# Optimization experiments

Measured on AMD Instinct MI355X. Metric: run time of the kernel, lower is better.

## Reference

```python
import jax, jax.numpy as jnp
import numpy as np

EPS = 1e-8  # torch CosineSimilarity default eps

def setup_inputs() -> dict:
    key = jax.random.key(0)
    kv, kt, k1, k2, k3, k4 = jax.random.split(key, 6)
    B, S = 16, 1024
    VD, TD, H = 1024, 768, 512
    visual_features = jax.random.normal(kv, (B, S, VD), dtype=jnp.float32)
    text_features = jax.random.normal(kt, (B, S, TD), dtype=jnp.float32)
    # nn.Linear params: weight [out, in], bias [out]
    Wv = jax.random.normal(k1, (H, VD), dtype=jnp.float32) * (1.0 / np.sqrt(VD))
    bv = jax.random.normal(k2, (H,), dtype=jnp.float32) * 0.01
    Wt = jax.random.normal(k3, (H, TD), dtype=jnp.float32) * (1.0 / np.sqrt(TD))
    bt = jax.random.normal(k4, (H,), dtype=jnp.float32) * 0.01
    return {"visual_features": visual_features, "text_features": text_features,
            "Wv": Wv, "bv": bv, "Wt": Wt, "bt": bt}

def reference(visual_features, text_features, Wv, bv, Wt, bt):
    # Linear projections
    v = jnp.einsum('bsd,hd->bsh', visual_features, Wv) + bv  # [B,S,H]
    t = jnp.einsum('bsd,hd->bsh', text_features, Wt) + bt    # [B,S,H]
    # Cosine similarity matrix via normalized batched GEMM
    # (algebraically equal to broadcasting CosineSimilarity over (B,S,S,H))
    dots = jnp.einsum('bih,bjh->bij', v, t)                   # [B,S,S]
    vn = jnp.linalg.norm(v, axis=-1)                          # [B,S]
    tn = jnp.linalg.norm(t, axis=-1)                          # [B,S]
    denom = jnp.maximum(vn[:, :, None] * tn[:, None, :], EPS)
    return dots / denom
```

## Files before the change

kernel.cpp:

```cpp
#include <hip/hip_runtime.h>
#include <hip/hip_bf16.h>

typedef __bf16 bf16x8 __attribute__((ext_vector_type(8)));
typedef __bf16 bf16x4 __attribute__((ext_vector_type(4)));
typedef float  f32x4  __attribute__((ext_vector_type(4)));

#define MFMA16(a, b, c) __builtin_amdgcn_mfma_f32_16x16x32_bf16((a), (b), (c), 0, 0, 0)

#define BATCH 16
#define SEQ   1024
#define VD    1024
#define TD    768
#define HDIM  512
#define MROWS (BATCH * SEQ)

typedef __attribute__((address_space(1))) const unsigned int gas_uint;
typedef __attribute__((address_space(3))) unsigned int las_uint;

__device__ __forceinline__ void async_copy16(const void* g, void* l) {
    __builtin_amdgcn_global_load_lds((gas_uint*)g, (las_uint*)l, 16, 0, 0);
}

__global__ __launch_bounds__(256) void wconv_kernel(const float* __restrict__ Wv,
                                                    const float* __restrict__ Wt,
                                                    __bf16* __restrict__ Wbv,
                                                    __bf16* __restrict__ Wbt) {
    const int NV = (HDIM * VD) / 4;
    const int NT = (HDIM * TD) / 4;
    int i = blockIdx.x * 256 + threadIdx.x;
    const float* src;
    __bf16* dst;
    if (i < NV) { src = Wv; dst = Wbv; }
    else        { i -= NV; if (i >= NT) return; src = Wt; dst = Wbt; }
    const float4 x = reinterpret_cast<const float4*>(src)[i];
    bf16x4 p = {(__bf16)x.x, (__bf16)x.y, (__bf16)x.z, (__bf16)x.w};
    reinterpret_cast<bf16x4*>(dst)[i] = p;
}

__global__ __launch_bounds__(256) void proj_kernel(
    const float* __restrict__ Xv, const __bf16* __restrict__ Wbv, const float* __restrict__ bv_,
    const float* __restrict__ Xt, const __bf16* __restrict__ Wbt, const float* __restrict__ bt_,
    __bf16* __restrict__ vout, __bf16* __restrict__ tout,
    float* __restrict__ vn2, float* __restrict__ tn2)
{
    const int L     = blockIdx.x;
    const int mlow  = L & 7;
    const int n     = (L >> 3) & 3;
    const int mhigh = (L >> 5) & 15;
    const int z     = L >> 9;
    const int m0    = (mhigh * 8 + mlow) * 128;
    const int n0    = n * 128;

    const float* X; const __bf16* Wb; const float* bias; __bf16* out; float* n2; int K;
    if (z == 0) { X = Xv; Wb = Wbv; bias = bv_; out = vout; n2 = vn2; K = VD; }
    else        { X = Xt; Wb = Wbt; bias = bt_; out = tout; n2 = tn2; K = TD; }

    __shared__ float  As[128 * 32];
    __shared__ __bf16 Bs[128 * 32];

    const int tid  = threadIdx.x;
    const int lane = tid & 63;
    const int wave = tid >> 6;
    const int wr   = wave >> 1;
    const int wc   = wave & 1;
    const int fr   = lane & 15;
    const int fq   = lane >> 4;

    f32x4 acc[4][4] = {};

    const int nk = K >> 5;
    for (int ki = 0; ki < nk; ++ki) {
        const int kk = ki << 5;

#pragma unroll
        for (int i = 0; i < 4; ++i) {
            const int c = i * 256 + tid;
            const int r = c >> 3;
            const int g = (c & 7) ^ (r & 7);
            async_copy16(&X[(size_t)(m0 + r) * K + kk + g * 4], &As[(c & ~63) * 4]);
        }
#pragma unroll
        for (int i = 0; i < 2; ++i) {
            const int c = i * 256 + tid;
            const int r = c >> 2;
            const int g = (c & 3) ^ (r & 3);
            async_copy16(&Wb[(size_t)(n0 + r) * K + kk + g * 8], &Bs[(c & ~63) * 8]);
        }
        __syncthreads();

        bf16x8 a[4], b[4];
#pragma unroll
        for (int tm = 0; tm < 4; ++tm) {
            const int r   = wr * 64 + tm * 16 + fr;
            const int key = r & 7;
            const f32x4 lo = *reinterpret_cast<const f32x4*>(&As[(r * 8 + ((fq * 2)     ^ key)) * 4]);
            const f32x4 hi = *reinterpret_cast<const f32x4*>(&As[(r * 8 + ((fq * 2 + 1) ^ key)) * 4]);
            bf16x8 av = {(__bf16)lo[0], (__bf16)lo[1], (__bf16)lo[2], (__bf16)lo[3],
                         (__bf16)hi[0], (__bf16)hi[1], (__bf16)hi[2], (__bf16)hi[3]};
            a[tm] = av;
        }
#pragma unroll
        for (int tn = 0; tn < 4; ++tn) {
            const int r = wc * 64 + tn * 16 + fr;
            b[tn] = *reinterpret_cast<const bf16x8*>(&Bs[(r * 4 + (fq ^ (r & 3))) * 8]);
        }
#pragma unroll
        for (int tm = 0; tm < 4; ++tm)
#pragma unroll
            for (int tn = 0; tn < 4; ++tn)
                acc[tm][tn] = MFMA16(a[tm], b[tn], acc[tm][tn]);
        __syncthreads();
    }

    float bc[4];
#pragma unroll
    for (int tn = 0; tn < 4; ++tn)
        bc[tn] = bias[n0 + wc * 64 + tn * 16 + fr];

#pragma unroll
    for (int tm = 0; tm < 4; ++tm) {
        const int rowb = m0 + wr * 64 + tm * 16 + fq * 4;
#pragma unroll
        for (int r = 0; r < 4; ++r) {
            float s = 0.f;
#pragma unroll
            for (int tn = 0; tn < 4; ++tn) {
                const float e = acc[tm][tn][r] + bc[tn];
                out[(size_t)(rowb + r) * HDIM + n0 + wc * 64 + tn * 16 + fr] = (__bf16)e;
                s = fmaf(e, e, s);
            }
            s += __shfl_xor(s, 1);
            s += __shfl_xor(s, 2);
            s += __shfl_xor(s, 4);
            s += __shfl_xor(s, 8);
            if (fr == 0) atomicAdd(&n2[rowb + r], s);
        }
    }
}

__global__ __launch_bounds__(256) void dots_kernel(const __bf16* __restrict__ v,
                                                   const __bf16* __restrict__ t,
                                                   const float* __restrict__ vn2,
                                                   const float* __restrict__ tn2,
                                                   float* __restrict__ out) {
    __shared__ __bf16 As[128 * 32];
    __shared__ __bf16 Bs[128 * 32];

    const int L  = blockIdx.x;
    const int b  = (L & 7) + ((L >> 9) << 3);
    const int j0 = ((L >> 3) & 7) * 128;
    const int i0 = ((L >> 6) & 7) * 128;

    const __bf16* vb = v + (size_t)b * SEQ * HDIM;
    const __bf16* tb = t + (size_t)b * SEQ * HDIM;

    const int tid  = threadIdx.x;
    const int lane = tid & 63;
    const int wave = tid >> 6;
    const int wr   = wave >> 1;
    const int wc   = wave & 1;
    const int fr   = lane & 15;
    const int fq   = lane >> 4;

    f32x4 acc[4][4] = {};

    for (int kk = 0; kk < HDIM; kk += 32) {
#pragma unroll
        for (int s = 0; s < 2; ++s) {
            const int c    = (wave * 2 + s) * 64 + lane;
            const int row  = c >> 2;
            const int part = c & 3;
            async_copy16(&vb[(size_t)(i0 + row) * HDIM + kk + part * 8],
                         &As[(wave * 2 + s) * 512]);
            async_copy16(&tb[(size_t)(j0 + row) * HDIM + kk + part * 8],
                         &Bs[(wave * 2 + s) * 512]);
        }
        __syncthreads();

        bf16x8 a[4], bfr[4];
#pragma unroll
        for (int t_ = 0; t_ < 4; ++t_) {
            a[t_]   = *reinterpret_cast<const bf16x8*>(&As[(wr * 64 + t_ * 16 + fr) * 32 + fq * 8]);
            bfr[t_] = *reinterpret_cast<const bf16x8*>(&Bs[(wc * 64 + t_ * 16 + fr) * 32 + fq * 8]);
        }
#pragma unroll
        for (int tm = 0; tm < 4; ++tm)
#pragma unroll
            for (int tn_ = 0; tn_ < 4; ++tn_)
                acc[tm][tn_] = MFMA16(a[tm], bfr[tn_], acc[tm][tn_]);
        __syncthreads();
    }

    float vr2[16];
#pragma unroll
    for (int tm = 0; tm < 4; ++tm)
#pragma unroll
        for (int r = 0; r < 4; ++r)
            vr2[tm * 4 + r] = vn2[b * SEQ + i0 + wr * 64 + tm * 16 + fq * 4 + r];

    float* outb = out + ((size_t)b << 20);
#pragma unroll
    for (int tn_ = 0; tn_ < 4; ++tn_) {
        const int j     = j0 + wc * 64 + tn_ * 16 + fr;
        const float tj2 = tn2[b * SEQ + j];
#pragma unroll
        for (int tm = 0; tm < 4; ++tm) {
            const int ib = i0 + wr * 64 + tm * 16 + fq * 4;
#pragma unroll
            for (int r = 0; r < 4; ++r) {
                const float denom = fmaxf(sqrtf(vr2[tm * 4 + r] * tj2), 1e-8f);
                outb[(size_t)(ib + r) * SEQ + j] = acc[tm][tn_][r] * __builtin_amdgcn_rcpf(denom);
            }
        }
    }
}

extern "C" void kernel_launch(void* const* d_in, const int* in_sizes, int n_in,
                              void* d_out, int out_size, void* d_ws, size_t ws_size,
                              hipStream_t stream) {
    const float* Xv = (const float*)d_in[0];
    const float* Xt = (const float*)d_in[1];
    const float* Wv = (const float*)d_in[2];
    const float* bv = (const float*)d_in[3];
    const float* Wt = (const float*)d_in[4];
    const float* bt = (const float*)d_in[5];
    float* out = (float*)d_out;

    char* ws = (char*)d_ws;
    size_t off = 0;
    __bf16* v   = (__bf16*)(ws + off); off += (size_t)MROWS * HDIM * 2;
    __bf16* t   = (__bf16*)(ws + off); off += (size_t)MROWS * HDIM * 2;
    __bf16* Wbv = (__bf16*)(ws + off); off += (size_t)HDIM * VD * 2;
    __bf16* Wbt = (__bf16*)(ws + off); off += (size_t)HDIM * TD * 2;
    float*  vn2 = (float*)(ws + off);  off += (size_t)MROWS * 4;
    float*  tn2 = (float*)(ws + off);  off += (size_t)MROWS * 4;

    hipMemsetAsync(vn2, 0, (size_t)2 * MROWS * 4, stream);

    wconv_kernel<<<896, 256, 0, stream>>>(Wv, Wt, Wbv, Wbt);

    proj_kernel<<<1024, 256, 0, stream>>>(Xv, Wbv, bv, Xt, Wbt, bt, v, t, vn2, tn2);

    dots_kernel<<<1024, 256, 0, stream>>>(v, t, vn2, tn2, out);
}
```

Baseline: 260.8 us.

## Pre-convert activations to bf16 and double-buffer GEMM tiles with BK=64

```diff
diff --git a/kernel.cpp b/kernel.cpp
--- a/kernel.cpp
+++ b/kernel.cpp
@@ -21,25 +21,51 @@
     __builtin_amdgcn_global_load_lds((gas_uint*)g, (las_uint*)l, 16, 0, 0);
 }
 
-__global__ __launch_bounds__(256) void wconv_kernel(const float* __restrict__ Wv,
-                                                    const float* __restrict__ Wt,
-                                                    __bf16* __restrict__ Wbv,
-                                                    __bf16* __restrict__ Wbt) {
-    const int NV = (HDIM * VD) / 4;
-    const int NT = (HDIM * TD) / 4;
+__device__ __forceinline__ void stage_tile_bf16(const __bf16* __restrict__ src,
+                                                size_t ld, int row0, int k0,
+                                                __bf16* __restrict__ buf, int tid) {
+#pragma unroll
+    for (int i = 0; i < 4; ++i) {
+        const int c = i * 256 + tid;
+        const int r = c >> 3;
+        const int g = (c & 7) ^ (r & 7);
+        async_copy16(&src[(size_t)(row0 + r) * ld + k0 + g * 8],
+                     &buf[(c & ~63) * 8]);
+    }
+}
+
+__device__ __forceinline__ bf16x8 frag_read(const __bf16* __restrict__ buf,
+                                            int r, int h, int fq) {
+    return *reinterpret_cast<const bf16x8*>(&buf[(r * 8 + ((h * 4 + fq) ^ (r & 7))) * 8]);
+}
+
+#define NC_XV (BATCH * SEQ * VD / 4)
+#define NC_XT (BATCH * SEQ * TD / 4)
+#define NC_WV (HDIM * VD / 4)
+#define NC_WT (HDIM * TD / 4)
+#define NC_TOTAL (NC_XV + NC_XT + NC_WV + NC_WT)
+
+__global__ __launch_bounds__(256) void conv_kernel(
+    const float* __restrict__ Xv, const float* __restrict__ Xt,
+    const float* __restrict__ Wv, const float* __restrict__ Wt,
+    __bf16* __restrict__ Xvb, __bf16* __restrict__ Xtb,
+    __bf16* __restrict__ Wvb, __bf16* __restrict__ Wtb) {
     int i = blockIdx.x * 256 + threadIdx.x;
+    if (i >= NC_TOTAL) return;
     const float* src;
     __bf16* dst;
-    if (i < NV) { src = Wv; dst = Wbv; }
-    else        { i -= NV; if (i >= NT) return; src = Wt; dst = Wbt; }
+    if (i < NC_XV)                     { src = Xv; dst = Xvb; }
+    else if ((i -= NC_XV) < NC_XT)     { src = Xt; dst = Xtb; }
+    else if ((i -= NC_XT) < NC_WV)     { src = Wv; dst = Wvb; }
+    else { i -= NC_WV;                   src = Wt; dst = Wtb; }
     const float4 x = reinterpret_cast<const float4*>(src)[i];
     bf16x4 p = {(__bf16)x.x, (__bf16)x.y, (__bf16)x.z, (__bf16)x.w};
     reinterpret_cast<bf16x4*>(dst)[i] = p;
 }
 
 __global__ __launch_bounds__(256) void proj_kernel(
-    const float* __restrict__ Xv, const __bf16* __restrict__ Wbv, const float* __restrict__ bv_,
-    const float* __restrict__ Xt, const __bf16* __restrict__ Wbt, const float* __restrict__ bt_,
+    const __bf16* __restrict__ Xvb, const __bf16* __restrict__ Wvb, const float* __restrict__ bv_,
+    const __bf16* __restrict__ Xtb, const __bf16* __restrict__ Wtb, const float* __restrict__ bt_,
     __bf16* __restrict__ vout, __bf16* __restrict__ tout,
     float* __restrict__ vn2, float* __restrict__ tn2)
 {
@@ -51,12 +77,12 @@
     const int m0    = (mhigh * 8 + mlow) * 128;
     const int n0    = n * 128;
 
-    const float* X; const __bf16* Wb; const float* bias; __bf16* out; float* n2; int K;
-    if (z == 0) { X = Xv; Wb = Wbv; bias = bv_; out = vout; n2 = vn2; K = VD; }
-    else        { X = Xt; Wb = Wbt; bias = bt_; out = tout; n2 = tn2; K = TD; }
-
-    __shared__ float  As[128 * 32];
-    __shared__ __bf16 Bs[128 * 32];
+    const __bf16* X; const __bf16* Wb; const float* bias; __bf16* out; float* n2; int K;
+    if (z == 0) { X = Xvb; Wb = Wvb; bias = bv_; out = vout; n2 = vn2; K = VD; }
+    else        { X = Xtb; Wb = Wtb; bias = bt_; out = tout; n2 = tn2; K = TD; }
+
+    __shared__ __bf16 As[2][128 * 64];
+    __shared__ __bf16 Bs[2][128 * 64];
 
     const int tid  = threadIdx.x;
     const int lane = tid & 63;
@@ -67,48 +93,35 @@
     const int fq   = lane >> 4;
 
     f32x4 acc[4][4] = {};
-
-    const int nk = K >> 5;
+    const int nk = K >> 6;
+
+    stage_tile_bf16(X,  K, m0, 0, As[0], tid);
+    stage_tile_bf16(Wb, K, n0, 0, Bs[0], tid);
+    __syncthreads();
+
     for (int ki = 0; ki < nk; ++ki) {
-        const int kk = ki << 5;
-
-#pragma unroll
-        for (int i = 0; i < 4; ++i) {
-            const int c = i * 256 + tid;
-            const int r = c >> 3;
-            const int g = (c & 7) ^ (r & 7);
-            async_copy16(&X[(size_t)(m0 + r) * K + kk + g * 4], &As[(c & ~63) * 4]);
-        }
-#pragma unroll
-        for (int i = 0; i < 2; ++i) {
-            const int c = i * 256 + tid;
-            const int r = c >> 2;
-            const int g = (c & 3) ^ (r & 3);
-            async_copy16(&Wb[(size_t)(n0 + r) * K + kk + g * 8], &Bs[(c & ~63) * 8]);
-        }
-        __syncthreads();
-
-        bf16x8 a[4], b[4];
-#pragma unroll
-        for (int tm = 0; tm < 4; ++tm) {
-            const int r   = wr * 64 + tm * 16 + fr;
-            const int key = r & 7;
-            const f32x4 lo = *reinterpret_cast<const f32x4*>(&As[(r * 8 + ((fq * 2)     ^ key)) * 4]);
-            const f32x4 hi = *reinterpret_cast<const f32x4*>(&As[(r * 8 + ((fq * 2 + 1) ^ key)) * 4]);
-            bf16x8 av = {(__bf16)lo[0], (__bf16)lo[1], (__bf16)lo[2], (__bf16)lo[3],
-                         (__bf16)hi[0], (__bf16)hi[1], (__bf16)hi[2], (__bf16)hi[3]};
-            a[tm] = av;
-        }
-#pragma unroll
-        for (int tn = 0; tn < 4; ++tn) {
-            const int r = wc * 64 + tn * 16 + fr;
-            b[tn] = *reinterpret_cast<const bf16x8*>(&Bs[(r * 4 + (fq ^ (r & 3))) * 8]);
-        }
-#pragma unroll
-        for (int tm = 0; tm < 4; ++tm)
+        if (ki + 1 < nk) {
+            const int kk = (ki + 1) << 6;
+            stage_tile_bf16(X,  K, m0, kk, As[(ki + 1) & 1], tid);
+            stage_tile_bf16(Wb, K, n0, kk, Bs[(ki + 1) & 1], tid);
+        }
+        const __bf16* Ab = As[ki & 1];
+        const __bf16* Bb = Bs[ki & 1];
+#pragma unroll
+        for (int h = 0; h < 2; ++h) {
+            bf16x8 a[4], b[4];
+#pragma unroll
+            for (int tm = 0; tm < 4; ++tm)
+                a[tm] = frag_read(Ab, wr * 64 + tm * 16 + fr, h, fq);
 #pragma unroll
             for (int tn = 0; tn < 4; ++tn)
-                acc[tm][tn] = MFMA16(a[tm], b[tn], acc[tm][tn]);
+                b[tn] = frag_read(Bb, wc * 64 + tn * 16 + fr, h, fq);
+#pragma unroll
+            for (int tm = 0; tm < 4; ++tm)
+#pragma unroll
+                for (int tn = 0; tn < 4; ++tn)
+                    acc[tm][tn] = MFMA16(a[tm], b[tn], acc[tm][tn]);
+        }
         __syncthreads();
     }
 
@@ -143,8 +156,8 @@
                                                    const float* __restrict__ vn2,
                                                    const float* __restrict__ tn2,
                                                    float* __restrict__ out) {
-    __shared__ __bf16 As[128 * 32];
-    __shared__ __bf16 Bs[128 * 32];
+    __shared__ __bf16 As[2][128 * 64];
+    __shared__ __bf16 Bs[2][128 * 64];
 
     const int L  = blockIdx.x;
     const int b  = (L & 7) + ((L >> 9) << 3);
@@ -163,31 +176,35 @@
     const int fq   = lane >> 4;
 
     f32x4 acc[4][4] = {};
-
-    for (int kk = 0; kk < HDIM; kk += 32) {
-#pragma unroll
-        for (int s = 0; s < 2; ++s) {
-            const int c    = (wave * 2 + s) * 64 + lane;
-            const int row  = c >> 2;
-            const int part = c & 3;
-            async_copy16(&vb[(size_t)(i0 + row) * HDIM + kk + part * 8],
-                         &As[(wave * 2 + s) * 512]);
-            async_copy16(&tb[(size_t)(j0 + row) * HDIM + kk + part * 8],
-                         &Bs[(wave * 2 + s) * 512]);
-        }
-        __syncthreads();
-
-        bf16x8 a[4], bfr[4];
-#pragma unroll
-        for (int t_ = 0; t_ < 4; ++t_) {
-            a[t_]   = *reinterpret_cast<const bf16x8*>(&As[(wr * 64 + t_ * 16 + fr) * 32 + fq * 8]);
-            bfr[t_] = *reinterpret_cast<const bf16x8*>(&Bs[(wc * 64 + t_ * 16 + fr) * 32 + fq * 8]);
-        }
-#pragma unroll
-        for (int tm = 0; tm < 4; ++tm)
-#pragma unroll
-            for (int tn_ = 0; tn_ < 4; ++tn_)
-                acc[tm][tn_] = MFMA16(a[tm], bfr[tn_], acc[tm][tn_]);
+    const int nk = HDIM >> 6;
+
+    stage_tile_bf16(vb, HDIM, i0, 0, As[0], tid);
+    stage_tile_bf16(tb, HDIM, j0, 0, Bs[0], tid);
+    __syncthreads();
+
+    for (int ki = 0; ki < nk; ++ki) {
+        if (ki + 1 < nk) {
+            const int kk = (ki + 1) << 6;
+            stage_tile_bf16(vb, HDIM, i0, kk, As[(ki + 1) & 1], tid);
+            stage_tile_bf16(tb, HDIM, j0, kk, Bs[(ki + 1) & 1], tid);
+        }
+        const __bf16* Ab = As[ki & 1];
+        const __bf16* Bb = Bs[ki & 1];
+#pragma unroll
+        for (int h = 0; h < 2; ++h) {
+            bf16x8 a[4], bfr[4];
+#pragma unroll
+            for (int tm = 0; tm < 4; ++tm)
+                a[tm] = frag_read(Ab, wr * 64 + tm * 16 + fr, h, fq);
+#pragma unroll
+            for (int tn = 0; tn < 4; ++tn)
+                bfr[tn] = frag_read(Bb, wc * 64 + tn * 16 + fr, h, fq);
+#pragma unroll
+            for (int tm = 0; tm < 4; ++tm)
+#pragma unroll
+                for (int tn = 0; tn < 4; ++tn)
+                    acc[tm][tn] = MFMA16(a[tm], bfr[tn], acc[tm][tn]);
+        }
         __syncthreads();
     }
 
@@ -200,8 +217,8 @@
 
     float* outb = out + ((size_t)b << 20);
 #pragma unroll
-    for (int tn_ = 0; tn_ < 4; ++tn_) {
-        const int j     = j0 + wc * 64 + tn_ * 16 + fr;
+    for (int tn = 0; tn < 4; ++tn) {
+        const int j     = j0 + wc * 64 + tn * 16 + fr;
         const float tj2 = tn2[b * SEQ + j];
 #pragma unroll
         for (int tm = 0; tm < 4; ++tm) {
@@ -209,7 +226,7 @@
 #pragma unroll
             for (int r = 0; r < 4; ++r) {
                 const float denom = fmaxf(sqrtf(vr2[tm * 4 + r] * tj2), 1e-8f);
-                outb[(size_t)(ib + r) * SEQ + j] = acc[tm][tn_][r] * __builtin_amdgcn_rcpf(denom);
+                outb[(size_t)(ib + r) * SEQ + j] = acc[tm][tn][r] * __builtin_amdgcn_rcpf(denom);
             }
         }
     }
@@ -230,16 +247,18 @@
     size_t off = 0;
     __bf16* v   = (__bf16*)(ws + off); off += (size_t)MROWS * HDIM * 2;
     __bf16* t   = (__bf16*)(ws + off); off += (size_t)MROWS * HDIM * 2;
-    __bf16* Wbv = (__bf16*)(ws + off); off += (size_t)HDIM * VD * 2;
-    __bf16* Wbt = (__bf16*)(ws + off); off += (size_t)HDIM * TD * 2;
+    __bf16* Xvb = (__bf16*)(ws + off); off += (size_t)MROWS * VD * 2;
+    __bf16* Xtb = (__bf16*)(ws + off); off += (size_t)MROWS * TD * 2;
+    __bf16* Wvb = (__bf16*)(ws + off); off += (size_t)HDIM * VD * 2;
+    __bf16* Wtb = (__bf16*)(ws + off); off += (size_t)HDIM * TD * 2;
     float*  vn2 = (float*)(ws + off);  off += (size_t)MROWS * 4;
     float*  tn2 = (float*)(ws + off);  off += (size_t)MROWS * 4;
 
     hipMemsetAsync(vn2, 0, (size_t)2 * MROWS * 4, stream);
 
-    wconv_kernel<<<896, 256, 0, stream>>>(Wv, Wt, Wbv, Wbt);
-
-    proj_kernel<<<1024, 256, 0, stream>>>(Xv, Wbv, bv, Xt, Wbt, bt, v, t, vn2, tn2);
+    conv_kernel<<<(NC_TOTAL + 255) / 256, 256, 0, stream>>>(Xv, Xt, Wv, Wt, Xvb, Xtb, Wvb, Wtb);
+
+    proj_kernel<<<1024, 256, 0, stream>>>(Xvb, Wvb, bv, Xtb, Wtb, bt, v, t, vn2, tn2);
 
     dots_kernel<<<1024, 256, 0, stream>>>(v, t, vn2, tn2, out);
 }
```

After: 248.3 us. 4.8% less time.
